# Performance work log

Measured on AMD Instinct MI355X. Metric: run time of the kernel, lower is better.

The kernel has to match this reference:

```python
import jax, jax.numpy as jnp
import numpy as np

STEP, LEAK = 16, 32
KS = STEP + LEAK          # kernel_size = 48
FODEP = KS                # forced depression window
SYNAPSES, NEURONS = 64, 256
IC, OC = 1, 10
DENSE = 0.5
THETA = DENSE * SYNAPSES * IC   # 32.0
BIAS = 0.5
BATCH, TIME = 16, 512


def setup_inputs() -> dict:
    key = jax.random.key(0)
    k1, k2 = jax.random.split(key)
    # binary input spikes, density 0.2
    input_spikes = (jax.random.uniform(k1, (BATCH, IC, SYNAPSES, TIME)) < 0.2).astype(jnp.float32)
    # weight ~ Exponential(rate=1/w_init=2).sample().clip(0,1), mean 0.5
    u = jax.random.uniform(k2, (OC * NEURONS, IC * SYNAPSES), minval=1e-6, maxval=1.0)
    weight = jnp.clip(-0.5 * jnp.log(u), 0.0, 1.0)
    return {"input_spikes": input_spikes, "weight": weight}


def _step_fire_leak_kernel(weight):
    # kernel[o, i, t] = max(0, min(t/step, -(t - w*step)/leak + w)), flipped on t
    t = jnp.arange(KS, dtype=weight.dtype)
    t_spike = t / STEP                                        # rising edge
    t_leak = -(t - weight[..., None] * STEP) / LEAK + weight[..., None]  # decaying edge
    kernel = jnp.maximum(jnp.zeros((), weight.dtype), jnp.minimum(t_spike, t_leak))
    return kernel[..., ::-1]


def _forward(input_spikes, weight):
    B, C, S, T = input_spikes.shape
    x = input_spikes.reshape(B, C * S, T)
    kernel = _step_fire_leak_kernel(weight)                   # [OC*N, IC*S, KS]
    # conv1d with padding = kernel_size on both sides -> T' = T + KS + 1
    pot = jax.lax.conv_general_dilated(
        x, kernel, window_strides=(1,), padding=[(KS, KS)],
        dimension_numbers=("NCH", "OIH", "NCH"))
    Tp = pot.shape[-1]
    pot = pot.reshape(B, OC, NEURONS, Tp) + BIAS * THETA      # unsupervised bias path

    # winner-takes-all scan over time with per-(batch, neuron) depression counter
    pot_t = pot.transpose(3, 0, 2, 1)                         # [T', B, N, OC]
    dep0 = jnp.zeros((B, NEURONS, OC), jnp.int32)

    def step_fn(dep, p):
        masked = jnp.where(dep == 0, p, jnp.zeros((), p.dtype))
        winner = jnp.argmax(masked, axis=-1)                  # [B, N]
        wpot = jnp.take_along_axis(masked, winner[..., None], axis=-1)[..., 0]
        spike = (wpot > THETA).astype(p.dtype)                # [B, N]
        w_t = jax.nn.one_hot(winner, OC, dtype=p.dtype) * spike[..., None]
        dep = jnp.clip(dep + spike.astype(jnp.int32)[..., None] * FODEP - 1, 0, FODEP - 1)
        return dep, w_t

    _, winners = jax.lax.scan(step_fn, dep0, pot_t)           # [T', B, N, OC]
    return winners.transpose(1, 3, 2, 0)                      # [B, OC, N, T'] float


def reference(input_spikes, weight):
    return _forward(input_spikes, weight)
```

## Files before the change

### kernel.cpp

```cpp
#include <hip/hip_runtime.h>

#define B_   16
#define OC_  10
#define N_   256
#define O_   2560
#define S_   64
#define T_   512
#define KS_  48
#define TP_  561
#define TT   24
#define WROW 72

#define XROWS 624
#define SCH    16
#define CPITCH 572
#define KP     18

#define OUTF4  5744640

using i32x4 = __attribute__((ext_vector_type(4))) int;

__global__ void prep_all(const float* __restrict__ x, const float* __restrict__ w,
                         unsigned char* __restrict__ xb, signed char* __restrict__ Bg,
                         float* __restrict__ outz) {
    if (blockIdx.x < 512) {
#pragma unroll
        for (int it = 0; it < 4; ++it) {
            int idx = blockIdx.x * 256 + threadIdx.x + it * 131072;
            int t = idx & 511;
            int bi = idx >> 9;
            int i = bi & 63, b = bi >> 6;
            xb[((size_t)(b * 512 + t) << 6) + i] = (x[idx] != 0.0f) ? 1 : 0;
        }
    } else if (blockIdx.x < 2432) {
        int base = (blockIdx.x - 512) * 256 + threadIdx.x;
#pragma unroll
        for (int it = 0; it < 16; ++it) {
            int idx = base + it * 491520;
            int i = idx & 63;
            int oj = idx >> 6;
            int j = oj % KS_, o = oj / KS_;
            float wv = w[(o << 6) + i];
            float rise = (float)j * 0.0625f;
            float leak = -((float)j - wv * 16.0f) * 0.03125f + wv;
            float kv   = fmaxf(0.0f, fminf(rise, leak));
            int q  = (int)lrintf(kv * 4194304.0f);
            int d0 = ((q + 128) & 255) - 128;
            int q1 = (q - d0) >> 8;
            int d1 = ((q1 + 128) & 255) - 128;
            int d2 = (q1 - d1) >> 8;
            int oc = o >> 4, ol = o & 15;
            int jm = j & 15, jh = j >> 4;
            int pos = jm * 3 + jh;
            size_t bse = (((size_t)(oc * KS_ + pos) * 48) + ol) * 64 + i;
            Bg[bse]            = (signed char)d0;
            Bg[bse + 16 * 64]  = (signed char)d1;
            Bg[bse + 32 * 64]  = (signed char)d2;
        }
    } else {
        i32x4* o4 = (i32x4*)outz;
        int base = (blockIdx.x - 2432) * 256 + threadIdx.x;
#pragma unroll
        for (int it = 0; it < 8; ++it) {
            int idx = base + it * 737280;
            if (idx < OUTF4) o4[idx] = (i32x4){0, 0, 0, 0};
        }
    }
}

__global__ __launch_bounds__(512, 2) void gemm_scan(
    const unsigned char* __restrict__ xb,
    const signed char*  __restrict__ Bg,
    float* __restrict__ out)
{
    __shared__ __align__(16) unsigned char smem[143616];
    unsigned char* xT    = smem;
    unsigned char* codeW = smem;
    float*         keyBB = (float*)(smem + 39936);
    unsigned char* codeBB = smem + 39936 + 82944;

    const int tid  = threadIdx.x;
    const int lane = tid & 63;
    const int wave = tid >> 6;
    const int tq   = wave >> 1;
    const int chh  = wave & 1;
    const int nc = blockIdx.x;
    const int b  = blockIdx.y;
    const int lrow = lane & 15;
    const int quad = lane >> 4;
    const int tw = tq * 144;

    float*         keyB  = keyBB + chh * (576 * KP);
    unsigned char* codeB = codeBB + chh * (576 * KP);

    const size_t SL = (size_t)KS_ * 48 * 64;
    const signed char* Bcur = Bg + (size_t)(chh * 80 + nc) * SL
                            + lrow * 64 + quad * 16;

    for (int z = tid; z < 112 * 4; z += 512) {
        int zi = z >> 2, p = z & 3;
        int r = (zi < 49) ? zi : (561 + zi - 49);
        *(i32x4*)(xT + r * 64 + p * 16) = (i32x4){0, 0, 0, 0};
    }
    const unsigned char* xbb = xb + ((size_t)b << 15);
    for (int q = tid; q < 2048; q += 512) {
        i32x4 v = *(const i32x4*)(xbb + q * 16);
        int t = q >> 2, p = q & 3;
        int r = 49 + t;
        *(i32x4*)(xT + r * 64 + ((p ^ ((r >> 1) & 3)) << 4)) = v;
    }

    i32x4 acc[9][3];
    i32x4 af[11], bfA[9], bfB[9];

#pragma unroll
    for (int jh = 0; jh < 3; ++jh)
#pragma unroll
        for (int f = 0; f < 3; ++f)
            bfA[jh * 3 + f] = *(const i32x4*)(Bcur + jh * 3072 + f * 1024);

    __syncthreads();

    {
        const int rb0 = tw + 16 + lrow;
        const int ca0 = ((quad ^ ((rb0 >> 1) & 3)) << 4);
#pragma unroll
        for (int k = 0; k < 11; ++k)
            af[k] = *(const i32x4*)(xT + (rb0 + k * 16) * 64 + ca0);
    }

#define MF(bfC, mi, jh, f)                                                    \
    acc[mi][f] = __builtin_amdgcn_mfma_i32_16x16x64_i8(                       \
        af[(mi) + 2 - (jh)], bfC[(jh) * 3 + (f)], acc[mi][f], 0, 0, 0)

#define PAIR(bfC, m0)                                                         \
    MF(bfC, m0, 0, 0); MF(bfC, m0, 0, 1); MF(bfC, m0, 0, 2);                  \
    MF(bfC, (m0)+1, 0, 0); MF(bfC, (m0)+1, 0, 1); MF(bfC, (m0)+1, 0, 2);      \
    MF(bfC, m0, 1, 0); MF(bfC, m0, 1, 1); MF(bfC, m0, 1, 2);                  \
    MF(bfC, (m0)+1, 1, 0); MF(bfC, (m0)+1, 1, 1); MF(bfC, (m0)+1, 1, 2);      \
    MF(bfC, m0, 2, 0); MF(bfC, m0, 2, 1); MF(bfC, m0, 2, 2);                  \
    MF(bfC, (m0)+1, 2, 0); MF(bfC, (m0)+1, 2, 1); MF(bfC, (m0)+1, 2, 2);

#define PAIR9(bfC)                                                            \
    MF(bfC, 8, 0, 0); MF(bfC, 8, 0, 1); MF(bfC, 8, 0, 2);                     \
    MF(bfC, 8, 1, 0); MF(bfC, 8, 1, 1); MF(bfC, 8, 1, 2);                     \
    MF(bfC, 8, 2, 0); MF(bfC, 8, 2, 1); MF(bfC, 8, 2, 2);

#define LDA_(row) (*(const i32x4*)(xT + (row) * 64 + coffN))
#define LDB_(BP, jh, f) (*(const i32x4*)((BP) + (tn3 + (jh)) * 3072 + (f) * 1024))

#define TLOC(T, bfC, bfN, BP) {                                               \
        const int rbn   = tw + 16 - (((T) + 1) & 15) + lrow;                  \
        const int coffN = ((quad ^ ((rbn >> 1) & 3)) << 4);                   \
        const int tn3   = (((T) + 1) & 15) * 3;                               \
        __builtin_amdgcn_s_setprio(1);                                        \
        PAIR(bfC, 0)                                                          \
        af[0] = LDA_(rbn);        af[1] = LDA_(rbn + 16);                     \
        bfN[0] = LDB_(BP, 0, 0); bfN[1] = LDB_(BP, 0, 1); bfN[2] = LDB_(BP, 0, 2); \
        PAIR(bfC, 2)                                                          \
        af[2] = LDA_(rbn + 32);   af[3] = LDA_(rbn + 48);                     \
        bfN[3] = LDB_(BP, 1, 0); bfN[4] = LDB_(BP, 1, 1); bfN[5] = LDB_(BP, 1, 2); \
        PAIR(bfC, 4)                                                          \
        af[4] = LDA_(rbn + 64);   af[5] = LDA_(rbn + 80);                     \
        bfN[6] = LDB_(BP, 2, 0); bfN[7] = LDB_(BP, 2, 1); bfN[8] = LDB_(BP, 2, 2); \
        PAIR(bfC, 6)                                                          \
        af[6] = LDA_(rbn + 96);   af[7] = LDA_(rbn + 112);                    \
        PAIR9(bfC)                                                            \
        af[8] = LDA_(rbn + 128);  af[9] = LDA_(rbn + 144);                    \
        af[10] = LDA_(rbn + 160);                                             \
        __builtin_amdgcn_s_setprio(0);                                        \
    }

    for (int c = 0; c < 5; ++c) {
        const signed char* Bnxt = (c == 4) ? Bcur : (Bcur + 16 * SL);

#pragma unroll
        for (int mi = 0; mi < 9; ++mi)
#pragma unroll
            for (int f = 0; f < 3; ++f)
                acc[mi][f] = (i32x4){0, 0, 0, 0};

        for (int tp = 0; tp < 7; ++tp) {
            TLOC(2 * tp,     bfA, bfB, Bcur)
            TLOC(2 * tp + 1, bfB, bfA, Bcur)
        }
        TLOC(14, bfA, bfB, Bcur)
        TLOC(15, bfB, bfA, Bnxt)

        {
            const unsigned char cv = (unsigned char)(chh * 5 + c + 1);
#pragma unroll
            for (int mi = 0; mi < 9; ++mi) {
#pragma unroll
                for (int r = 0; r < 4; ++r) {
                    int t = tw + mi * 16 + quad * 4 + r;
                    int pq_i = acc[mi][0][r] + (acc[mi][1][r] << 8)
                             + (acc[mi][2][r] << 16);
                    float pq = (float)pq_i * 2.384185791015625e-7f;
                    int ix = t * KP + lrow;
                    if (c == 0) {
                        keyB[ix] = pq; codeB[ix] = cv;
                    } else if (pq > keyB[ix]) {
                        keyB[ix] = pq; codeB[ix] = cv;
                    }
                }
            }
        }
        Bcur = Bnxt;
    }

#undef MF
#undef PAIR
#undef PAIR9
#undef LDA_
#undef LDB_
#undef TLOC

    __syncthreads();

    for (int ix = tid; ix < 576 * 16; ix += 512) {
        int t = ix >> 4, nl = ix & 15;
        if (t >= TP_) continue;
        int ip = t * KP + nl;
        float f0 = keyBB[ip];
        float f1 = keyBB[576 * KP + ip];
        float best = f0;
        unsigned char cd = codeBB[ip];
        if (f1 > f0) { best = f1; cd = codeBB[576 * KP + ip]; }
        codeW[nl * CPITCH + t] = ((best + 16.0f) > 32.0f) ? cd : (unsigned char)0;
    }
    __syncthreads();

    {
        const int ln = tid & 63;
        float* ob = out + (((size_t)b * OC_) * N_ + nc * SCH) * TP_;
        for (int nsel = wave; nsel < SCH; nsel += 8) {
            const unsigned char* cp = &codeW[nsel * CPITCH];
            int t = 0;
            while (t < TP_) {
                int tt = t + ln;
                unsigned char v = (tt < TP_) ? cp[tt] : (unsigned char)0;
                unsigned long long mask = __ballot(v != 0);
                if (mask == 0ULL) { t += 64; continue; }
                int k = (int)__builtin_ctzll(mask);
                if (ln == k)
                    ob[((size_t)(v - 1) * N_ + nsel) * TP_ + (t + k)] = 1.0f;
                t += k + KS_;
            }
        }
    }
}

__global__ void transpose_w(const float* __restrict__ w, float* __restrict__ wT) {
    int idx = blockIdx.x * 256 + threadIdx.x;
    if (idx >= O_ * S_) return;
    int o = idx >> 6, i = idx & 63;
    wT[i * O_ + o] = w[idx];
}

__global__ __launch_bounds__(256) void conv_kernel(
    const float* __restrict__ x, const float* __restrict__ wT,
    float* __restrict__ pot)
{
    const int b  = blockIdx.y;
    const int t0 = blockIdx.z * TT;
    const int o  = blockIdx.x * 256 + threadIdx.x;

    __shared__ __align__(16) float xsh[S_][WROW];
    for (int idx = threadIdx.x; idx < S_ * WROW; idx += 256) {
        int i = idx / WROW, m = idx - i * WROW;
        int t = t0 - KS_ + m;
        float v = 0.0f;
        if (t >= 0 && t < T_) v = x[(b * S_ + i) * T_ + t];
        xsh[i][m] = v;
    }
    __syncthreads();

    float acch[TT], accl[TT];
#pragma unroll
    for (int tl = 0; tl < TT; ++tl) { acch[tl] = 0.0f; accl[tl] = 0.0f; }

    for (int i = 0; i < S_; ++i) {
        float xw[WROW];
#pragma unroll
        for (int w4 = 0; w4 < WROW / 4; ++w4) {
            const float4 v = *reinterpret_cast<const float4*>(&xsh[i][w4 * 4]);
            xw[w4 * 4 + 0] = v.x; xw[w4 * 4 + 1] = v.y;
            xw[w4 * 4 + 2] = v.z; xw[w4 * 4 + 3] = v.w;
        }
        const float wv = wT[i * O_ + o];
#pragma unroll
        for (int j = 1; j < KS_; ++j) {
            float rise = (float)j * 0.0625f;
            float leak = -((float)j - wv * 16.0f) * 0.03125f + wv;
            float kv   = fmaxf(0.0f, fminf(rise, leak));
            float khi  = rintf(kv * 4096.0f) * 2.44140625e-4f;
            float klo  = kv - khi;
#pragma unroll
            for (int tl = 0; tl < TT; ++tl) {
                float xv = xw[tl + (KS_ - 1) - j];
                acch[tl] = fmaf(xv, khi, acch[tl]);
                accl[tl] = fmaf(xv, klo, accl[tl]);
            }
        }
    }
#pragma unroll
    for (int tl = 0; tl < TT; ++tl) {
        int t = t0 + tl;
        if (t < TP_) pot[((size_t)b * TP_ + t) * O_ + o] = acch[tl] + accl[tl];
    }
}

__global__ void scan_prep(const float* __restrict__ pot, unsigned char* __restrict__ code) {
    int idx = blockIdx.x * 256 + threadIdx.x;
    if (idx >= B_ * TP_ * N_) return;
    int n  = idx & (N_ - 1);
    int bt = idx >> 8;
    const float* p = pot + (size_t)bt * O_ + n;
    float best = p[0]; int bo = 0;
#pragma unroll
    for (int oc = 1; oc < OC_; ++oc) {
        float v = p[oc * N_];
        if (v > best) { best = v; bo = oc; }
    }
    code[idx] = ((best + 16.0f) > 32.0f) ? (unsigned char)(bo + 1) : (unsigned char)0;
}

__global__ void scan_run(const unsigned char* __restrict__ code, float* __restrict__ out) {
    int idx = blockIdx.x * 256 + threadIdx.x;
    if (idx >= B_ * N_) return;
    int b = idx >> 8, n = idx & 255;
    const unsigned char* c = code + (size_t)b * TP_ * N_ + n;
    int t = 0;
    while (t < TP_) {
        unsigned char buf[KS_];
#pragma unroll
        for (int k = 0; k < KS_; ++k) {
            int tt = t + k;
            buf[k] = (tt < TP_) ? c[(size_t)tt * N_] : (unsigned char)0;
        }
        int adv = KS_;
#pragma unroll
        for (int k = 0; k < KS_; ++k) {
            if (buf[k]) {
                out[(((size_t)b * OC_ + (buf[k] - 1)) * N_ + n) * TP_ + (t + k)] = 1.0f;
                adv = k + KS_;
                break;
            }
        }
        t += adv;
    }
}

extern "C" void kernel_launch(void* const* d_in, const int* in_sizes, int n_in,
                              void* d_out, int out_size, void* d_ws, size_t ws_size,
                              hipStream_t stream) {
    const float* x = (const float*)d_in[0];
    const float* w = (const float*)d_in[1];
    float* out = (float*)d_out;

    char* ws = (char*)d_ws;
    const size_t szX = (size_t)B_ * T_ * S_;
    const size_t szB = (size_t)160 * KS_ * 48 * 64;
    const size_t need = szX + szB;

    if (ws_size >= need) {
        unsigned char* xb  = (unsigned char*)ws;
        signed char* Bg    = (signed char*)(ws + szX);

        prep_all<<<5312, 256, 0, stream>>>(x, w, xb, Bg, out);
        gemm_scan<<<dim3(16, 16), 512, 0, stream>>>(xb, Bg, out);
    } else {
        size_t pot_bytes  = (size_t)B_ * TP_ * O_ * sizeof(float);
        size_t code_bytes = (size_t)B_ * TP_ * N_;
        float* pot = (float*)ws;
        unsigned char* code = (unsigned char*)(ws + pot_bytes);
        float* wT = (float*)(ws + pot_bytes + code_bytes);

        hipMemsetAsync(d_out, 0, (size_t)out_size * sizeof(float), stream);
        transpose_w<<<(O_ * S_ + 255) / 256, 256, 0, stream>>>(w, wT);
        conv_kernel<<<dim3(O_ / 256, B_, (TP_ + TT - 1) / TT), 256, 0, stream>>>(x, wT, pot);
        scan_prep<<<(B_ * TP_ * N_ + 255) / 256, 256, 0, stream>>>(pot, code);
        scan_run<<<(B_ * N_ + 255) / 256, 256, 0, stream>>>(code, out);
    }
}
```

Baseline: 229.1 us.

## Give each wave two output channels over a narrower time strip, dropping cross-wave channel split

```diff
diff --git a/kernel.cpp b/kernel.cpp
--- a/kernel.cpp
+++ b/kernel.cpp
@@ -11,7 +11,7 @@
 #define TT   24
 #define WROW 72
 
-#define XROWS 624
+#define XROWS 688
 #define SCH    16
 #define CPITCH 572
 #define KP     18
@@ -73,31 +73,33 @@
     const signed char*  __restrict__ Bg,
     float* __restrict__ out)
 {
-    __shared__ __align__(16) unsigned char smem[143616];
+    __shared__ __align__(16) unsigned char smem[44032 + 41472 + 10368];
     unsigned char* xT    = smem;
     unsigned char* codeW = smem;
-    float*         keyBB = (float*)(smem + 39936);
-    unsigned char* codeBB = smem + 39936 + 82944;
+    float*         keyB  = (float*)(smem + 44032);
+    unsigned char* codeB = smem + 44032 + 41472;
 
     const int tid  = threadIdx.x;
     const int lane = tid & 63;
     const int wave = tid >> 6;
-    const int tq   = wave >> 1;
-    const int chh  = wave & 1;
     const int nc = blockIdx.x;
     const int b  = blockIdx.y;
     const int lrow = lane & 15;
     const int quad = lane >> 4;
-    const int tw = tq * 144;
-
-    float*         keyB  = keyBB + chh * (576 * KP);
-    unsigned char* codeB = codeBB + chh * (576 * KP);
+    const int tw = wave * 80;
 
     const size_t SL = (size_t)KS_ * 48 * 64;
-    const signed char* Bcur = Bg + (size_t)(chh * 80 + nc) * SL
-                            + lrow * 64 + quad * 16;
-
-    for (int z = tid; z < 112 * 4; z += 512) {
+    const signed char* Bc = Bg + (size_t)nc * SL + lrow * 64 + quad * 16;
+
+#pragma unroll
+    for (int mi = 0; mi < 5; ++mi)
+#pragma unroll
+        for (int r = 0; r < 4; ++r) {
+            int t_ = tw + mi * 16 + quad * 4 + r;
+            if (t_ < 576) keyB[t_ * KP + lrow] = -1.0e30f;
+        }
+
+    for (int z = tid; z < 176 * 4; z += 512) {
         int zi = z >> 2, p = z & 3;
         int r = (zi < 49) ? zi : (561 + zi - 49);
         *(i32x4*)(xT + r * 64 + p * 16) = (i32x4){0, 0, 0, 0};
@@ -110,14 +112,16 @@
         *(i32x4*)(xT + r * 64 + ((p ^ ((r >> 1) & 3)) << 4)) = v;
     }
 
-    i32x4 acc[9][3];
-    i32x4 af[11], bfA[9], bfB[9];
+    i32x4 acc0[5][3], acc1[5][3];
+    i32x4 af[7], bf0[9], bf1[9];
 
 #pragma unroll
     for (int jh = 0; jh < 3; ++jh)
 #pragma unroll
-        for (int f = 0; f < 3; ++f)
-            bfA[jh * 3 + f] = *(const i32x4*)(Bcur + jh * 3072 + f * 1024);
+        for (int f = 0; f < 3; ++f) {
+            bf0[jh * 3 + f] = *(const i32x4*)(Bc + jh * 3072 + f * 1024);
+            bf1[jh * 3 + f] = *(const i32x4*)(Bc + 16 * SL + jh * 3072 + f * 1024);
+        }
 
     __syncthreads();
 
@@ -125,96 +129,125 @@
         const int rb0 = tw + 16 + lrow;
         const int ca0 = ((quad ^ ((rb0 >> 1) & 3)) << 4);
 #pragma unroll
-        for (int k = 0; k < 11; ++k)
+        for (int k = 0; k < 7; ++k)
             af[k] = *(const i32x4*)(xT + (rb0 + k * 16) * 64 + ca0);
     }
 
-#define MF(bfC, mi, jh, f)                                                    \
-    acc[mi][f] = __builtin_amdgcn_mfma_i32_16x16x64_i8(                       \
-        af[(mi) + 2 - (jh)], bfC[(jh) * 3 + (f)], acc[mi][f], 0, 0, 0)
-
-#define PAIR(bfC, m0)                                                         \
-    MF(bfC, m0, 0, 0); MF(bfC, m0, 0, 1); MF(bfC, m0, 0, 2);                  \
-    MF(bfC, (m0)+1, 0, 0); MF(bfC, (m0)+1, 0, 1); MF(bfC, (m0)+1, 0, 2);      \
-    MF(bfC, m0, 1, 0); MF(bfC, m0, 1, 1); MF(bfC, m0, 1, 2);                  \
-    MF(bfC, (m0)+1, 1, 0); MF(bfC, (m0)+1, 1, 1); MF(bfC, (m0)+1, 1, 2);      \
-    MF(bfC, m0, 2, 0); MF(bfC, m0, 2, 1); MF(bfC, m0, 2, 2);                  \
-    MF(bfC, (m0)+1, 2, 0); MF(bfC, (m0)+1, 2, 1); MF(bfC, (m0)+1, 2, 2);
-
-#define PAIR9(bfC)                                                            \
-    MF(bfC, 8, 0, 0); MF(bfC, 8, 0, 1); MF(bfC, 8, 0, 2);                     \
-    MF(bfC, 8, 1, 0); MF(bfC, 8, 1, 1); MF(bfC, 8, 1, 2);                     \
-    MF(bfC, 8, 2, 0); MF(bfC, 8, 2, 1); MF(bfC, 8, 2, 2);
+#define MFX(CH, mi, jh, f)                                                    \
+    acc##CH[mi][f] = __builtin_amdgcn_mfma_i32_16x16x64_i8(                   \
+        af[(mi) + 2 - (jh)], bf##CH[(jh) * 3 + (f)], acc##CH[mi][f], 0, 0, 0)
+
+#define MF6(mi, jh)                                                           \
+    MFX(0, mi, jh, 0); MFX(0, mi, jh, 1); MFX(0, mi, jh, 2);                  \
+    MFX(1, mi, jh, 0); MFX(1, mi, jh, 1); MFX(1, mi, jh, 2);
 
 #define LDA_(row) (*(const i32x4*)(xT + (row) * 64 + coffN))
-#define LDB_(BP, jh, f) (*(const i32x4*)((BP) + (tn3 + (jh)) * 3072 + (f) * 1024))
-
-#define TLOC(T, bfC, bfN, BP) {                                               \
-        const int rbn   = tw + 16 - (((T) + 1) & 15) + lrow;                  \
+#define LDB0_(jh, f) (*(const i32x4*)(Bc + (tn3 + (jh)) * 3072 + (f) * 1024))
+#define LDB1_(jh, f) (*(const i32x4*)(Bc + 16 * SL + (tn3 + (jh)) * 3072 + (f) * 1024))
+
+#define TLOC(T) {                                                             \
+        const int tn  = (T) + 1;                                              \
+        const int rbn = tw + 16 - tn + lrow;                                  \
         const int coffN = ((quad ^ ((rbn >> 1) & 3)) << 4);                   \
-        const int tn3   = (((T) + 1) & 15) * 3;                               \
-        __builtin_amdgcn_s_setprio(1);                                        \
-        PAIR(bfC, 0)                                                          \
-        af[0] = LDA_(rbn);        af[1] = LDA_(rbn + 16);                     \
-        bfN[0] = LDB_(BP, 0, 0); bfN[1] = LDB_(BP, 0, 1); bfN[2] = LDB_(BP, 0, 2); \
-        PAIR(bfC, 2)                                                          \
-        af[2] = LDA_(rbn + 32);   af[3] = LDA_(rbn + 48);                     \
-        bfN[3] = LDB_(BP, 1, 0); bfN[4] = LDB_(BP, 1, 1); bfN[5] = LDB_(BP, 1, 2); \
-        PAIR(bfC, 4)                                                          \
-        af[4] = LDA_(rbn + 64);   af[5] = LDA_(rbn + 80);                     \
-        bfN[6] = LDB_(BP, 2, 0); bfN[7] = LDB_(BP, 2, 1); bfN[8] = LDB_(BP, 2, 2); \
-        PAIR(bfC, 6)                                                          \
-        af[6] = LDA_(rbn + 96);   af[7] = LDA_(rbn + 112);                    \
-        PAIR9(bfC)                                                            \
-        af[8] = LDA_(rbn + 128);  af[9] = LDA_(rbn + 144);                    \
-        af[10] = LDA_(rbn + 160);                                             \
-        __builtin_amdgcn_s_setprio(0);                                        \
-    }
-
-    for (int c = 0; c < 5; ++c) {
-        const signed char* Bnxt = (c == 4) ? Bcur : (Bcur + 16 * SL);
-
-#pragma unroll
-        for (int mi = 0; mi < 9; ++mi)
-#pragma unroll
-            for (int f = 0; f < 3; ++f)
-                acc[mi][f] = (i32x4){0, 0, 0, 0};
-
-        for (int tp = 0; tp < 7; ++tp) {
-            TLOC(2 * tp,     bfA, bfB, Bcur)
-            TLOC(2 * tp + 1, bfB, bfA, Bcur)
-        }
-        TLOC(14, bfA, bfB, Bcur)
-        TLOC(15, bfB, bfA, Bnxt)
+        const int tn3 = tn * 3;                                               \
+        __builtin_amdgcn_s_setprio(1);                                        \
+        MF6(0,0) MF6(1,0) MF6(2,0) MF6(3,0) MF6(4,0)                          \
+        __builtin_amdgcn_s_setprio(0);                                        \
+        af[6] = LDA_(rbn + 96);                                               \
+        bf0[0]=LDB0_(0,0); bf0[1]=LDB0_(0,1); bf0[2]=LDB0_(0,2);              \
+        bf1[0]=LDB1_(0,0); bf1[1]=LDB1_(0,1); bf1[2]=LDB1_(0,2);              \
+        __builtin_amdgcn_s_setprio(1);                                        \
+        MF6(0,1) MF6(1,1) MF6(2,1) MF6(3,1) MF6(4,1)                          \
+        __builtin_amdgcn_s_setprio(0);                                        \
+        af[5] = LDA_(rbn + 80);                                               \
+        bf0[3]=LDB0_(1,0); bf0[4]=LDB0_(1,1); bf0[5]=LDB0_(1,2);              \
+        bf1[3]=LDB1_(1,0); bf1[4]=LDB1_(1,1); bf1[5]=LDB1_(1,2);              \
+        __builtin_amdgcn_s_setprio(1);                                        \
+        MF6(0,2) af[0] = LDA_(rbn);                                           \
+        MF6(1,2) af[1] = LDA_(rbn + 16);                                      \
+        MF6(2,2) af[2] = LDA_(rbn + 32);                                      \
+        MF6(3,2) af[3] = LDA_(rbn + 48);                                      \
+        MF6(4,2) af[4] = LDA_(rbn + 64);                                      \
+        __builtin_amdgcn_s_setprio(0);                                        \
+        bf0[6]=LDB0_(2,0); bf0[7]=LDB0_(2,1); bf0[8]=LDB0_(2,2);              \
+        bf1[6]=LDB1_(2,0); bf1[7]=LDB1_(2,1); bf1[8]=LDB1_(2,2);              \
+    }
+
+#define TLOCF {                                                               \
+        const int rbn = tw + 16 + lrow;                                       \
+        const int coffN = ((quad ^ ((rbn >> 1) & 3)) << 4);                   \
+        __builtin_amdgcn_s_setprio(1);                                        \
+        MF6(0,0) MF6(1,0) MF6(2,0) MF6(3,0) MF6(4,0)                          \
+        __builtin_amdgcn_s_setprio(0);                                        \
+        af[6] = LDA_(rbn + 96);                                               \
+        __builtin_amdgcn_s_setprio(1);                                        \
+        MF6(0,1) MF6(1,1) MF6(2,1) MF6(3,1) MF6(4,1)                          \
+        __builtin_amdgcn_s_setprio(0);                                        \
+        af[5] = LDA_(rbn + 80);                                               \
+        __builtin_amdgcn_s_setprio(1);                                        \
+        MF6(0,2) af[0] = LDA_(rbn);                                           \
+        MF6(1,2) af[1] = LDA_(rbn + 16);                                      \
+        MF6(2,2) af[2] = LDA_(rbn + 32);                                      \
+        MF6(3,2) af[3] = LDA_(rbn + 48);                                      \
+        MF6(4,2) af[4] = LDA_(rbn + 64);                                      \
+        __builtin_amdgcn_s_setprio(0);                                        \
+    }
+
+    for (int p = 0; p < 5; ++p) {
+#pragma unroll
+        for (int mi = 0; mi < 5; ++mi)
+#pragma unroll
+            for (int f = 0; f < 3; ++f) {
+                acc0[mi][f] = (i32x4){0, 0, 0, 0};
+                acc1[mi][f] = (i32x4){0, 0, 0, 0};
+            }
+
+#pragma unroll
+        for (int T = 0; T < 15; ++T) TLOC(T)
+        TLOCF
+
+        if (p < 4) {
+            Bc += 32 * SL;
+#pragma unroll
+            for (int jh = 0; jh < 3; ++jh)
+#pragma unroll
+                for (int f = 0; f < 3; ++f) {
+                    bf0[jh * 3 + f] = *(const i32x4*)(Bc + jh * 3072 + f * 1024);
+                    bf1[jh * 3 + f] = *(const i32x4*)(Bc + 16 * SL + jh * 3072 + f * 1024);
+                }
+        }
 
         {
-            const unsigned char cv = (unsigned char)(chh * 5 + c + 1);
-#pragma unroll
-            for (int mi = 0; mi < 9; ++mi) {
+            const unsigned char cv0 = (unsigned char)(2 * p + 1);
+            const unsigned char cv1 = (unsigned char)(2 * p + 2);
+#pragma unroll
+            for (int mi = 0; mi < 5; ++mi) {
 #pragma unroll
                 for (int r = 0; r < 4; ++r) {
-                    int t = tw + mi * 16 + quad * 4 + r;
-                    int pq_i = acc[mi][0][r] + (acc[mi][1][r] << 8)
-                             + (acc[mi][2][r] << 16);
-                    float pq = (float)pq_i * 2.384185791015625e-7f;
-                    int ix = t * KP + lrow;
-                    if (c == 0) {
-                        keyB[ix] = pq; codeB[ix] = cv;
-                    } else if (pq > keyB[ix]) {
-                        keyB[ix] = pq; codeB[ix] = cv;
+                    int t_ = tw + mi * 16 + quad * 4 + r;
+                    if (t_ < 576) {
+                        int ix = t_ * KP + lrow;
+                        int q0 = acc0[mi][0][r] + (acc0[mi][1][r] << 8)
+                               + (acc0[mi][2][r] << 16);
+                        float p0 = (float)q0 * 2.384185791015625e-7f;
+                        if (p0 > keyB[ix]) { keyB[ix] = p0; codeB[ix] = cv0; }
+                        int q1 = acc1[mi][0][r] + (acc1[mi][1][r] << 8)
+                               + (acc1[mi][2][r] << 16);
+                        float p1 = (float)q1 * 2.384185791015625e-7f;
+                        if (p1 > keyB[ix]) { keyB[ix] = p1; codeB[ix] = cv1; }
                     }
                 }
             }
         }
-        Bcur = Bnxt;
-    }
-
-#undef MF
-#undef PAIR
-#undef PAIR9
+    }
+
+#undef MFX
+#undef MF6
 #undef LDA_
-#undef LDB_
+#undef LDB0_
+#undef LDB1_
 #undef TLOC
+#undef TLOCF
 
     __syncthreads();
 
@@ -222,11 +255,8 @@
         int t = ix >> 4, nl = ix & 15;
         if (t >= TP_) continue;
         int ip = t * KP + nl;
-        float f0 = keyBB[ip];
-        float f1 = keyBB[576 * KP + ip];
-        float best = f0;
-        unsigned char cd = codeBB[ip];
-        if (f1 > f0) { best = f1; cd = codeBB[576 * KP + ip]; }
+        float best = keyB[ip];
+        unsigned char cd = codeB[ip];
         codeW[nl * CPITCH + t] = ((best + 16.0f) > 32.0f) ? cd : (unsigned char)0;
     }
     __syncthreads();
```

Measured after the change: 336.4 us. 46.8% more time.
